# Optimization experiments

Hardware: AMD Instinct MI355X
Metric: run time of the kernel (lower is better)

The kernel has to match this reference:

```python
import jax, jax.numpy as jnp
import numpy as np

B, S, D, H, DH, M = 4, 4096, 1024, 16, 64, 128


def _create_projection_matrix(m, d, seed=0):
    # Block-orthogonal Gaussian projection (FAVOR+), same math as the numpy helper.
    np.random.seed(seed)
    n_block = m // d
    blocks = []
    for _ in range(n_block):
        block = np.random.normal(0, 1, (d, d))
        q, _ = np.linalg.qr(block)
        blocks.append(q.T)
    rem = m - n_block * d
    if rem > 0:
        block = np.random.normal(0, 1, (d, d))
        q, _ = np.linalg.qr(block)
        blocks.append(q.T[:rem])
    proj = np.vstack(blocks)
    multiplier = np.linalg.norm(np.random.normal(0, 1, (m, d)), axis=1)
    return (np.diag(multiplier) @ proj).astype(np.float32)


def setup_inputs() -> dict:
    key = jax.random.key(0)
    ks = jax.random.split(key, 8)
    lim_attn = np.sqrt(6.0 / (D + H * DH)).astype(np.float32)
    lim_out = np.sqrt(6.0 / (H * DH + D)).astype(np.float32)
    head_pos = np.linspace(0.0 + 1.0 / (2.0 * H), 1.0, H, endpoint=False, dtype=np.float32).reshape(1, 1, H, 1)
    return {
        "source_input": jax.random.normal(ks[0], (B, S, D), jnp.float32),
        "pos_ft": jax.random.normal(ks[1], (B, S, D), jnp.float32),
        "pos_ft_slopes": jax.random.normal(ks[2], (B, S, D), jnp.float32),
        "value_weight": jax.random.uniform(ks[3], (D, H, DH), jnp.float32, -lim_attn, lim_attn),
        "pos_ft_weight": jax.random.uniform(ks[4], (D, H, DH), jnp.float32, -lim_attn, lim_attn),
        "pos_ft_scale": jnp.ones((1, 1, H, 1), jnp.float32),
        "pos_ft_offsets": jnp.asarray(head_pos),
        "output_weight": jax.random.uniform(ks[5], (H * DH, D), jnp.float32, -lim_out, lim_out),
        "projection_matrix": jnp.asarray(_create_projection_matrix(M, DH, seed=1234)),
    }


def _fourier_features(x, projection_matrix):
    # x: [b, l, h, d] -> [b, l, h, 2m]
    d = x.shape[-1]
    m = projection_matrix.shape[0]
    data_normalizer = 1.0 / (float(d) ** 0.25)
    ratio = 1.0 / (float(m) ** 0.5)
    xd = jnp.einsum('blhd,md->blhm', data_normalizer * x, projection_matrix)
    xd = jnp.clip(xd, -10000.0, 10000.0)
    return jnp.concatenate([ratio * jnp.sin(xd), ratio * jnp.cos(xd)], axis=-1)


def reference(source_input, pos_ft, pos_ft_slopes, value_weight, pos_ft_weight,
              pos_ft_scale, pos_ft_offsets, output_weight, projection_matrix):
    # Projections
    value = jnp.einsum('bnm,mhd->bnhd', source_input, value_weight)        # [B,S,H,DH]
    pos_proj = jnp.einsum('bnm,mhd->bnhd', pos_ft, pos_ft_weight)          # [B,S,H,DH]
    slope_proj = jnp.einsum('bnm,mhd->bnhd', pos_ft_slopes, pos_ft_weight) # [B,S,H,DH]

    query_pos = pos_ft_scale * pos_proj
    key_pos = query_pos + pos_ft_offsets * (pos_ft_scale * slope_proj)

    # FAVOR fourier random features
    q_prime = _fourier_features(query_pos, projection_matrix)  # [B,S,H,2M]
    k_prime = _fourier_features(key_pos, projection_matrix)    # [B,S,H,2M]

    # Linear attention: O(L) kvs accumulation (non-causal, normalize_attn=False)
    kvs = jnp.einsum('blhm,blhd->bhmd', k_prime, value)         # [B,H,2M,DH]
    av = jnp.einsum('blhm,bhmd->blhd', q_prime, kvs)            # [B,S,H,DH]

    slen = av.shape[1]
    norms = jnp.linalg.norm(slope_proj, axis=-1, keepdims=True) / float(slen)
    av = norms * av

    out = jnp.einsum('bnm,md->bnd', av.reshape(av.shape[0], slen, -1), output_weight)
    # Dropout is identity at inference (training=False)
    return out
```

## Files before the change

kernel.cpp:

```cpp
#include <hip/hip_runtime.h>
#include <math.h>


typedef unsigned short u16;
typedef __attribute__((ext_vector_type(8))) short bf16x8;
typedef __attribute__((ext_vector_type(4))) float floatx4;

__device__ __forceinline__ float bf2f(u16 u) {
  union { unsigned int i; float f; } v; v.i = ((unsigned int)u) << 16; return v.f;
}
__device__ __forceinline__ u16 f2bf(float f) {
  union { float f; unsigned int i; } v; v.f = f;
  unsigned int r = v.i + 0x7fffu + ((v.i >> 16) & 1u);
  return (u16)(r >> 16);
}
__device__ __forceinline__ bool wire_f32(const unsigned* probe) {
  return probe[0] == 0x3F800000u;
}
__device__ __forceinline__ void gload_lds16(const void* g, void* l) {
  __builtin_amdgcn_global_load_lds(
      (const __attribute__((address_space(1))) void*)g,
      (__attribute__((address_space(3))) void*)l, 16, 0, 0);
}

__device__ __forceinline__ void gemm_body(
    const u16* __restrict__ A, int lda, const u16* __restrict__ B, int ldb,
    void* __restrict__ C, long coff, int Klog, int fold, int ofmt, bool f32w,
    long m0, long n0, u16* sA, u16* sB)
{
  const int t = threadIdx.x;
  const int wave = t >> 6, lane = t & 63;
  const int ll = lane & 15, quad = lane >> 4;
  const int wm0 = (wave >> 1) * 64, wn0 = (wave & 1) * 64;
  const int lr = lane >> 2, lc = (lane & 3) * 8;
  floatx4 acc[4][4];
  floatx4 zero = {0.0f, 0.0f, 0.0f, 0.0f};
  #pragma unroll
  for (int i = 0; i < 4; i++)
    #pragma unroll
    for (int j = 0; j < 4; j++) acc[i][j] = zero;

  for (int kc = 0; kc < Klog; kc += 32) {
    int akc = kc, bkc = kc;
    if (fold) {
      akc = (kc < 1024) ? kc : kc - 1024;
      bkc = (kc < 2048) ? kc : kc - 2048;
    }
    #pragma unroll
    for (int j = 0; j < 2; j++) {
      int r0 = wave * 32 + j * 16;
      gload_lds16(&A[(m0 + r0 + lr) * (long)lda + akc + lc], &sA[r0 * 32]);
      gload_lds16(&B[(n0 + r0 + lr) * (long)ldb + bkc + lc], &sB[r0 * 32]);
    }
    __syncthreads();
    bf16x8 af[4], bfr[4];
    #pragma unroll
    for (int i = 0; i < 4; i++) {
      af[i]  = *(const bf16x8*)&sA[(wm0 + i * 16 + ll) * 32 + quad * 8];
      bfr[i] = *(const bf16x8*)&sB[(wn0 + i * 16 + ll) * 32 + quad * 8];
    }
    #pragma unroll
    for (int i = 0; i < 4; i++)
      #pragma unroll
      for (int j = 0; j < 4; j++)
        acc[i][j] = __builtin_amdgcn_mfma_f32_16x16x32_bf16(af[i], bfr[j], acc[i][j], 0, 0, 0);
    __syncthreads();
  }
  #pragma unroll
  for (int i = 0; i < 4; i++)
    #pragma unroll
    for (int j = 0; j < 4; j++)
      #pragma unroll
      for (int r = 0; r < 4; r++) {
        long row = m0 + wm0 + i * 16 + quad * 4 + r;
        long col = n0 + wn0 + j * 16 + ll;
        float v = acc[i][j][r];
        long addr = coff + row * 1024 + col;
        if (ofmt == 0) ((u16*)C)[addr] = f2bf(v);
        else if (ofmt == 1) ((float*)C)[addr] = v;
        else if (f32w) ((float*)C)[addr] = v;
        else ((u16*)C)[addr] = f2bf(v);
      }
}

__global__ __launch_bounds__(256) void gemm_gl(
    const u16* __restrict__ A, int lda, const u16* __restrict__ B, int ldb,
    void* __restrict__ C, long coff, int Klog, int fold, int ofmt,
    const unsigned* __restrict__ probe)
{
  __shared__ u16 sA[128 * 32], sB[128 * 32];
  gemm_body(A, lda, B, ldb, C, coff, Klog, fold, ofmt, wire_f32(probe),
            (long)blockIdx.x * 128, (long)blockIdx.y * 128, sA, sB);
}

__global__ __launch_bounds__(256) void gemm_mega(
    const u16* __restrict__ A2, const u16* __restrict__ W2,
    float* __restrict__ posp, const u16* __restrict__ srcb,
    const u16* __restrict__ wvt, u16* __restrict__ vT,
    const unsigned* __restrict__ probe)
{
  __shared__ u16 pool[20480];
  const int id = blockIdx.x;
  const int xcd = id & 7, pos = id >> 3;
  const int t = threadIdx.x;
  const int wave = t >> 6, lane = t & 63;
  const int ll = lane & 15, quad = lane >> 4;
  const int wm0 = (wave >> 1) * 64, wn0 = (wave & 1) * 64;
  const int lr = lane >> 2, lc = (lane & 3) * 8;
  floatx4 acc[4][4];
  floatx4 zero = {0.0f, 0.0f, 0.0f, 0.0f};
  #pragma unroll
  for (int i = 0; i < 4; i++)
    #pragma unroll
    for (int j = 0; j < 4; j++) acc[i][j] = zero;

  if (pos < 64) {
    int tile = xcd * 64 + pos;
    long m0 = (long)(tile >> 3) * 128, n0 = (long)(tile & 7) * 128;
    u16* sAh = pool;
    u16* sAl = pool + 4096;
    u16* sBh = pool + 8192;
    u16* sBl = pool + 12288;
    for (int kc = 0; kc < 1024; kc += 32) {
      #pragma unroll
      for (int j = 0; j < 2; j++) {
        int r0 = wave * 32 + j * 16;
        gload_lds16(&A2[(m0 + r0 + lr) * 2048 + kc + lc],        &sAh[r0 * 32]);
        gload_lds16(&A2[(m0 + r0 + lr) * 2048 + 1024 + kc + lc], &sAl[r0 * 32]);
        gload_lds16(&W2[(n0 + r0 + lr) * 2048 + kc + lc],        &sBh[r0 * 32]);
        gload_lds16(&W2[(n0 + r0 + lr) * 2048 + 1024 + kc + lc], &sBl[r0 * 32]);
      }
      __syncthreads();
      bf16x8 ah[4], al[4], bh[4], bl[4];
      #pragma unroll
      for (int i = 0; i < 4; i++) {
        ah[i] = *(const bf16x8*)&sAh[(wm0 + i * 16 + ll) * 32 + quad * 8];
        al[i] = *(const bf16x8*)&sAl[(wm0 + i * 16 + ll) * 32 + quad * 8];
        bh[i] = *(const bf16x8*)&sBh[(wn0 + i * 16 + ll) * 32 + quad * 8];
        bl[i] = *(const bf16x8*)&sBl[(wn0 + i * 16 + ll) * 32 + quad * 8];
      }
      #pragma unroll
      for (int i = 0; i < 4; i++)
        #pragma unroll
        for (int j = 0; j < 4; j++) {
          acc[i][j] = __builtin_amdgcn_mfma_f32_16x16x32_bf16(ah[i], bh[j], acc[i][j], 0, 0, 0);
          acc[i][j] = __builtin_amdgcn_mfma_f32_16x16x32_bf16(ah[i], bl[j], acc[i][j], 0, 0, 0);
          acc[i][j] = __builtin_amdgcn_mfma_f32_16x16x32_bf16(al[i], bh[j], acc[i][j], 0, 0, 0);
        }
      __syncthreads();
    }
    #pragma unroll
    for (int i = 0; i < 4; i++)
      #pragma unroll
      for (int j = 0; j < 4; j++)
        #pragma unroll
        for (int r = 0; r < 4; r++) {
          long row = m0 + wm0 + i * 16 + quad * 4 + r;
          long col = n0 + wn0 + j * 16 + ll;
          posp[row * 1024 + col] = acc[i][j][r];
        }
  } else {
    int v = xcd * 32 + (pos - 64);
    long m0 = (long)(v >> 3) * 128, n0 = (long)(v & 7) * 128;
    u16* sA = pool;
    u16* sB = pool + 4096;
    for (int kc = 0; kc < 1024; kc += 32) {
      #pragma unroll
      for (int j = 0; j < 2; j++) {
        int r0 = wave * 32 + j * 16;
        gload_lds16(&srcb[(m0 + r0 + lr) * 1024 + kc + lc], &sA[r0 * 32]);
        gload_lds16(&wvt[(n0 + r0 + lr) * 1024 + kc + lc],  &sB[r0 * 32]);
      }
      __syncthreads();
      bf16x8 af[4], bfr[4];
      #pragma unroll
      for (int i = 0; i < 4; i++) {
        af[i]  = *(const bf16x8*)&sA[(wm0 + i * 16 + ll) * 32 + quad * 8];
        bfr[i] = *(const bf16x8*)&sB[(wn0 + i * 16 + ll) * 32 + quad * 8];
      }
      #pragma unroll
      for (int i = 0; i < 4; i++)
        #pragma unroll
        for (int j = 0; j < 4; j++)
          acc[i][j] = __builtin_amdgcn_mfma_f32_16x16x32_bf16(af[i], bfr[j], acc[i][j], 0, 0, 0);
      __syncthreads();
    }
    u16 (*sT)[136] = (u16(*)[136])pool;
    #pragma unroll
    for (int i = 0; i < 4; i++)
      #pragma unroll
      for (int j = 0; j < 4; j++)
        #pragma unroll
        for (int r = 0; r < 4; r++)
          sT[wn0 + j * 16 + ll][wm0 + i * 16 + quad * 4 + r] = f2bf(acc[i][j][r]);
    __syncthreads();
    for (int u = t; u < 2048; u += 256) {
      int d = u >> 4, c8 = (u & 15) * 8;
      *(uint4*)&vT[(n0 + d) * 4096 + m0 + c8] = *(const uint4*)&sT[d][c8];
    }
  }
}

__device__ __forceinline__ void split_body(
    const void* __restrict__ Aw, long aoff, u16* __restrict__ A2, int rowbase,
    bool f32w, long idx)
{
  int row = (int)(idx >> 7);
  int c8 = (int)(idx & 127) * 8;
  u16 h8[8], l8[8];
  if (f32w) {
    const float* ap = (const float*)Aw + aoff + (long)row * 1024 + c8;
    #pragma unroll
    for (int e = 0; e < 8; e++) {
      float v = ap[e]; u16 hb = f2bf(v);
      h8[e] = hb; l8[e] = f2bf(v - bf2f(hb));
    }
  } else {
    *(uint4*)h8 = *(const uint4*)((const u16*)Aw + aoff + (long)row * 1024 + c8);
    #pragma unroll
    for (int e = 0; e < 8; e++) l8[e] = 0;
  }
  u16* orow = A2 + (long)(rowbase + row) * 2048;
  *(uint4*)&orow[c8] = *(uint4*)h8;
  *(uint4*)&orow[1024 + c8] = *(uint4*)l8;
}

__device__ __forceinline__ void conv_body(
    const void* __restrict__ Aw, long aoff, u16* __restrict__ out,
    bool f32w, long idx)
{
  long base = idx * 8;
  u16 h8[8];
  if (f32w) {
    const float* ap = (const float*)Aw + aoff + base;
    #pragma unroll
    for (int e = 0; e < 8; e++) h8[e] = f2bf(ap[e]);
  } else {
    *(uint4*)h8 = *(const uint4*)((const u16*)Aw + aoff + base);
  }
  *(uint4*)&out[base] = *(uint4*)h8;
}

__global__ __launch_bounds__(256) void split_hilo(
    const void* __restrict__ Aw, long aoff, u16* __restrict__ A2, int rowbase,
    const unsigned* __restrict__ probe)
{
  split_body(Aw, aoff, A2, rowbase, wire_f32(probe),
             (long)blockIdx.x * 256 + threadIdx.x);
}

__global__ __launch_bounds__(256) void conv_bf16(
    const void* __restrict__ Aw, long aoff, u16* __restrict__ out,
    const unsigned* __restrict__ probe)
{
  conv_body(Aw, aoff, out, wire_f32(probe),
            (long)blockIdx.x * 256 + threadIdx.x);
}

__global__ __launch_bounds__(256) void mega2(
    const u16* __restrict__ av, const u16* __restrict__ wot,
    void* __restrict__ dout, long coff,
    const void* __restrict__ posf, const void* __restrict__ slpf,
    const void* __restrict__ src, long ioff_next,
    u16* __restrict__ A2, u16* __restrict__ srcb,
    const unsigned* __restrict__ probe)
{
  __shared__ u16 sA[128 * 32], sB[128 * 32];
  const bool f32w = wire_f32(probe);
  int id = blockIdx.x;
  if (id < 256) {
    int tile = (id & 7) * 32 + (id >> 3);
    gemm_body(av, 1024, wot, 1024, dout, coff, 1024, 0, 2, f32w,
              (long)(tile >> 3) * 128, (long)(tile & 7) * 128, sA, sB);
  } else if (id < 2304) {
    split_body(posf, ioff_next, A2, 0, f32w,
               (long)(id - 256) * 256 + threadIdx.x);
  } else if (id < 4352) {
    split_body(slpf, ioff_next, A2, 4096, f32w,
               (long)(id - 2304) * 256 + threadIdx.x);
  } else {
    conv_body(src, ioff_next, srcb, f32w,
              (long)(id - 4352) * 256 + threadIdx.x);
  }
}

__global__ __launch_bounds__(256) void transpose_w(
    const void* __restrict__ in, u16* __restrict__ outb,
    const unsigned* __restrict__ probe)
{
  __shared__ float s[64][65];
  const bool f32w = wire_f32(probe);
  int t = threadIdx.x;
  int r0 = blockIdx.y * 64, c0 = blockIdx.x * 64;
  for (int u = t; u < 4096; u += 256) {
    int r = u >> 6, c = u & 63;
    long idx = (long)(r0 + r) * 1024 + c0 + c;
    s[c][r] = f32w ? ((const float*)in)[idx] : bf2f(((const u16*)in)[idx]);
  }
  __syncthreads();
  for (int u = t; u < 4096; u += 256) {
    int r = u >> 6, c = u & 63;
    outb[(long)(c0 + r) * 1024 + r0 + c] = f2bf(s[r][c]);
  }
}

__global__ __launch_bounds__(256) void transpose_w2(
    const void* __restrict__ in, u16* __restrict__ out2,
    const unsigned* __restrict__ probe)
{
  __shared__ float s[64][65];
  const bool f32w = wire_f32(probe);
  int t = threadIdx.x;
  int r0 = blockIdx.y * 64, c0 = blockIdx.x * 64;
  for (int u = t; u < 4096; u += 256) {
    int r = u >> 6, c = u & 63;
    long idx = (long)(r0 + r) * 1024 + c0 + c;
    s[c][r] = f32w ? ((const float*)in)[idx] : bf2f(((const u16*)in)[idx]);
  }
  __syncthreads();
  for (int u = t; u < 4096; u += 256) {
    int r = u >> 6, c = u & 63;
    float v = s[r][c];
    u16 hb = f2bf(v);
    long rowb = (long)(c0 + r) * 2048;
    out2[rowb + r0 + c] = hb;
    out2[rowb + 1024 + r0 + c] = f2bf(v - bf2f(hb));
  }
}

__global__ __launch_bounds__(256) void proj_prep(
    const void* __restrict__ proj, u16* __restrict__ P2,
    const unsigned* __restrict__ probe)
{
  const bool f32w = wire_f32(probe);
  int idx = blockIdx.x * 256 + threadIdx.x;
  int m = idx >> 6, d = idx & 63;
  const float dn = 0.3535533905932738f;
  float v = dn * (f32w ? ((const float*)proj)[idx] : bf2f(((const u16*)proj)[idx]));
  u16 hb = f2bf(v);
  P2[(long)m * 128 + d] = hb;
  P2[(long)m * 128 + 64 + d] = f2bf(v - bf2f(hb));
}

__global__ __launch_bounds__(256) void featurize_mfma(
    const float* __restrict__ posp, const float* __restrict__ slpp,
    const u16* __restrict__ P2, const void* __restrict__ scl,
    const void* __restrict__ offs, u16* __restrict__ qp, u16* __restrict__ kpT,
    const unsigned* __restrict__ probe, int h0)
{
  __shared__ u16 sAp[4 * 64 * 32], sAs[4 * 64 * 32], sB[4 * 128 * 32];
  const bool f32w = wire_f32(probe);
  const int t = threadIdx.x;
  const int wave = t >> 6, lane = t & 63;
  const int ll = lane & 15, quad = lane >> 4;
  const int wm0 = (wave >> 1) * 32, wn0 = (wave & 1) * 64;
  const int g = blockIdx.y, h = h0 + g;
  const int l0 = blockIdx.x * 64;
  const float s1 = f32w ? ((const float*)scl)[h] : bf2f(((const u16*)scl)[h]);
  const float s2 = (f32w ? ((const float*)offs)[h] : bf2f(((const u16*)offs)[h])) * s1;
  const float ratio = 0.08838834764831845f;

  for (int u = t; u < 512; u += 256) {
    int r = u >> 3, cc = u & 7;
    const float* pp = posp + (long)(l0 + r) * 1024 + h * 64 + cc * 8;
    const float* sp = slpp + (long)(l0 + r) * 1024 + h * 64 + cc * 8;
    u16 ph[8], pl[8], sh[8], sl[8];
    #pragma unroll
    for (int e = 0; e < 8; e++) {
      float vp = pp[e]; u16 hb = f2bf(vp);
      ph[e] = hb; pl[e] = f2bf(vp - bf2f(hb));
      float vs = sp[e]; u16 sb = f2bf(vs);
      sh[e] = sb; sl[e] = f2bf(vs - bf2f(sb));
    }
    int ch = cc >> 2, cw = (cc & 3) * 8;
    *(uint4*)&sAp[((ch) * 64 + r) * 32 + cw]     = *(uint4*)ph;
    *(uint4*)&sAp[((2 + ch) * 64 + r) * 32 + cw] = *(uint4*)pl;
    *(uint4*)&sAs[((ch) * 64 + r) * 32 + cw]     = *(uint4*)sh;
    *(uint4*)&sAs[((2 + ch) * 64 + r) * 32 + cw] = *(uint4*)sl;
  }
  for (int u = t; u < 2048; u += 256) {
    int r = u >> 4, q4 = u & 15;
    uint4 v = *(const uint4*)&P2[(long)r * 128 + q4 * 8];
    int ch = q4 >> 2, cw = (q4 & 3) * 8;
    *(uint4*)&sB[(ch * 128 + r) * 32 + cw] = v;
  }
  __syncthreads();

  floatx4 accp[2][4], accs[2][4];
  floatx4 zero = {0.0f, 0.0f, 0.0f, 0.0f};
  #pragma unroll
  for (int i = 0; i < 2; i++)
    #pragma unroll
    for (int j = 0; j < 4; j++) { accp[i][j] = zero; accs[i][j] = zero; }

  const int ACH[6] = {0, 1, 0, 1, 2, 3};
  const int BCH[6] = {0, 1, 2, 3, 0, 1};
  #pragma unroll
  for (int kci = 0; kci < 6; kci++) {
    int ac = ACH[kci], bc = BCH[kci];
    bf16x8 ap[2], as2[2], bfr[4];
    #pragma unroll
    for (int i = 0; i < 2; i++) {
      ap[i]  = *(const bf16x8*)&sAp[(ac * 64 + wm0 + i * 16 + ll) * 32 + quad * 8];
      as2[i] = *(const bf16x8*)&sAs[(ac * 64 + wm0 + i * 16 + ll) * 32 + quad * 8];
    }
    #pragma unroll
    for (int j = 0; j < 4; j++)
      bfr[j] = *(const bf16x8*)&sB[(bc * 128 + wn0 + j * 16 + ll) * 32 + quad * 8];
    #pragma unroll
    for (int i = 0; i < 2; i++)
      #pragma unroll
      for (int j = 0; j < 4; j++) {
        accp[i][j] = __builtin_amdgcn_mfma_f32_16x16x32_bf16(ap[i],  bfr[j], accp[i][j], 0, 0, 0);
        accs[i][j] = __builtin_amdgcn_mfma_f32_16x16x32_bf16(as2[i], bfr[j], accs[i][j], 0, 0, 0);
      }
  }

  #pragma unroll
  for (int i = 0; i < 2; i++) {
    int lbase = l0 + wm0 + i * 16 + quad * 4;
    #pragma unroll
    for (int j = 0; j < 4; j++) {
      int m = wn0 + j * 16 + ll;
      u16 ksin[4], kcos[4];
      #pragma unroll
      for (int r = 0; r < 4; r++) {
        float dq = s1 * accp[i][j][r];
        float dk = dq + s2 * accs[i][j][r];
        dq = fminf(fmaxf(dq, -10000.0f), 10000.0f);
        dk = fminf(fmaxf(dk, -10000.0f), 10000.0f);
        long qbase = ((long)g * 4096 + lbase + r) * 256;
        qp[qbase + m]       = f2bf(ratio * __sinf(dq));
        qp[qbase + m + 128] = f2bf(ratio * __cosf(dq));
        ksin[r] = f2bf(ratio * __sinf(dk));
        kcos[r] = f2bf(ratio * __cosf(dk));
      }
      *(uint2*)&kpT[((long)(g * 256 + m)) * 4096 + lbase]       = *(uint2*)ksin;
      *(uint2*)&kpT[((long)(g * 256 + m + 128)) * 4096 + lbase] = *(uint2*)kcos;
    }
  }
}

__global__ __launch_bounds__(256) void transpose_v(
    const u16* __restrict__ in, u16* __restrict__ out)
{
  __shared__ u16 s[64][72];
  int t = threadIdx.x;
  int c0 = blockIdx.x * 64;
  int r0 = blockIdx.y * 64;
  for (int u = t; u < 512; u += 256) {
    int r = u >> 3, c8 = (u & 7) * 8;
    uint4 v = *(const uint4*)&in[(long)(r0 + r) * 1024 + c0 + c8];
    const u16* pv = (const u16*)&v;
    #pragma unroll
    for (int e = 0; e < 8; e++) s[c8 + e][r] = pv[e];
  }
  __syncthreads();
  for (int u = t; u < 512; u += 256) {
    int r = u >> 3, c8 = (u & 7) * 8;
    *(uint4*)&out[(long)(c0 + r) * 4096 + r0 + c8] = *(const uint4*)&s[r][c8];
  }
}

__global__ __launch_bounds__(256) void norm_kernel(
    const float* __restrict__ slp, float* __restrict__ nrm)
{
  int idx = blockIdx.x * 256 + threadIdx.x;
  int row = idx >> 4, h = idx & 15;
  const float* p = slp + (long)row * 1024 + h * 64;
  float acc = 0.0f;
  #pragma unroll
  for (int i = 0; i < 16; i++) {
    float4 v = *(const float4*)&p[i * 4];
    acc += v.x * v.x + v.y * v.y + v.z * v.z + v.w * v.w;
  }
  nrm[idx] = sqrtf(acc) * (1.0f / 4096.0f);
}

__global__ __launch_bounds__(256) void kvs_mfma(
    const u16* __restrict__ kpT, const u16* __restrict__ vT,
    float* __restrict__ kvp, int h0)
{
  __shared__ u16 sA[256][40], sB[64][40];
  const int t = threadIdx.x;
  const int wave = t >> 6, lane = t & 63;
  const int ll = lane & 15, quad = lane >> 4;
  const int wm0 = wave * 64;
  const int ks = blockIdx.x, g = blockIdx.y;
  const int G = gridDim.y, KS = gridDim.x;
  const int h = h0 + g;
  const int lch = 4096 / KS;
  const int lbase = ks * lch;
  floatx4 acc[4][4];
  floatx4 zero = {0.0f, 0.0f, 0.0f, 0.0f};
  #pragma unroll
  for (int i = 0; i < 4; i++)
    #pragma unroll
    for (int j = 0; j < 4; j++) acc[i][j] = zero;

  for (int kc = 0; kc < lch; kc += 32) {
    for (int u = t; u < 1024; u += 256) {
      int r = u >> 2, s = u & 3;
      *(uint4*)&sA[r][s * 8] =
          *(const uint4*)&kpT[((long)(g * 256 + r)) * 4096 + lbase + kc + s * 8];
    }
    {
      int r = t >> 2, s = t & 3;
      if (t < 256)
        *(uint4*)&sB[r][s * 8] =
            *(const uint4*)&vT[((long)(h * 64 + r)) * 4096 + lbase + kc + s * 8];
    }
    __syncthreads();
    bf16x8 af[4], bfr[4];
    #pragma unroll
    for (int i = 0; i < 4; i++) {
      af[i] = *(const bf16x8*)&sA[wm0 + i * 16 + ll][quad * 8];
      bfr[i] = *(const bf16x8*)&sB[i * 16 + ll][quad * 8];
    }
    #pragma unroll
    for (int i = 0; i < 4; i++)
      #pragma unroll
      for (int j = 0; j < 4; j++)
        acc[i][j] = __builtin_amdgcn_mfma_f32_16x16x32_bf16(af[i], bfr[j], acc[i][j], 0, 0, 0);
    __syncthreads();
  }
  long obase = ((long)ks * G + g) * 256;
  #pragma unroll
  for (int i = 0; i < 4; i++)
    #pragma unroll
    for (int j = 0; j < 4; j++)
      #pragma unroll
      for (int r = 0; r < 4; r++) {
        int row = wm0 + i * 16 + quad * 4 + r;
        int col = j * 16 + ll;
        kvp[(obase + row) * 64 + col] = acc[i][j][r];
      }
}

__global__ __launch_bounds__(256) void kvs_reduce(
    const float* __restrict__ kvp, u16* __restrict__ kvsTh,
    u16* __restrict__ kvsTl, int G, int KS)
{
  int idx = blockIdx.x * 256 + threadIdx.x;
  int m = idx & 255, d = (idx >> 8) & 63, g = idx >> 14;
  float s = 0.0f;
  for (int p = 0; p < KS; p++)
    s += kvp[(((long)p * G + g) * 256 + m) * 64 + d];
  u16 hb = f2bf(s);
  long o = ((long)g * 64 + d) * 256 + m;
  kvsTh[o] = hb;
  kvsTl[o] = f2bf(s - bf2f(hb));
}

__global__ __launch_bounds__(256) void av_mfma(
    const u16* __restrict__ qp, const u16* __restrict__ kvsTh,
    const u16* __restrict__ kvsTl, const float* __restrict__ nrm,
    u16* __restrict__ av, int h0)
{
  __shared__ u16 sA[128][40], sBh[64][40], sBl[64][40];
  const int t = threadIdx.x;
  const int wave = t >> 6, lane = t & 63;
  const int ll = lane & 15, quad = lane >> 4;
  const int wm0 = wave * 32;
  const int g = blockIdx.y, h = h0 + g;
  const int l0 = blockIdx.x * 128;
  floatx4 acc[2][4];
  floatx4 zero = {0.0f, 0.0f, 0.0f, 0.0f};
  #pragma unroll
  for (int i = 0; i < 2; i++)
    #pragma unroll
    for (int j = 0; j < 4; j++) acc[i][j] = zero;

  for (int kc = 0; kc < 256; kc += 32) {
    for (int u = t; u < 512; u += 256) {
      int r = u >> 2, s = u & 3;
      *(uint4*)&sA[r][s * 8] =
          *(const uint4*)&qp[((long)g * 4096 + l0 + r) * 256 + kc + s * 8];
    }
    {
      int r = t >> 2, s4 = t & 3;
      long o = ((long)g * 64 + r) * 256 + kc + s4 * 8;
      *(uint4*)&sBh[r][s4 * 8] = *(const uint4*)&kvsTh[o];
      *(uint4*)&sBl[r][s4 * 8] = *(const uint4*)&kvsTl[o];
    }
    __syncthreads();
    bf16x8 af[2], bh[4], bl[4];
    #pragma unroll
    for (int i = 0; i < 2; i++)
      af[i] = *(const bf16x8*)&sA[wm0 + i * 16 + ll][quad * 8];
    #pragma unroll
    for (int j = 0; j < 4; j++) {
      bh[j] = *(const bf16x8*)&sBh[j * 16 + ll][quad * 8];
      bl[j] = *(const bf16x8*)&sBl[j * 16 + ll][quad * 8];
    }
    #pragma unroll
    for (int i = 0; i < 2; i++)
      #pragma unroll
      for (int j = 0; j < 4; j++) {
        acc[i][j] = __builtin_amdgcn_mfma_f32_16x16x32_bf16(af[i], bh[j], acc[i][j], 0, 0, 0);
        acc[i][j] = __builtin_amdgcn_mfma_f32_16x16x32_bf16(af[i], bl[j], acc[i][j], 0, 0, 0);
      }
    __syncthreads();
  }
  #pragma unroll
  for (int i = 0; i < 2; i++)
    #pragma unroll
    for (int r = 0; r < 4; r++) {
      int l = l0 + wm0 + i * 16 + quad * 4 + r;
      float nv = nrm[l * 16 + h];
      #pragma unroll
      for (int j = 0; j < 4; j++) {
        int d = j * 16 + ll;
        av[(long)l * 1024 + h * 64 + d] = f2bf(acc[i][j][r] * nv);
      }
    }
}

extern "C" void kernel_launch(void* const* d_in, const int* in_sizes, int n_in,
                              void* d_out, int out_size, void* d_ws, size_t ws_size,
                              hipStream_t stream) {
  const void* src  = d_in[0];
  const void* posf = d_in[1];
  const void* slpf = d_in[2];
  const void* wv   = d_in[3];
  const void* wp   = d_in[4];
  const void* scl  = d_in[5];
  const void* offs = d_in[6];
  const void* wo   = d_in[7];
  const void* proj = d_in[8];
  const unsigned* probe = (const unsigned*)d_in[5];
  char* ws = (char*)d_ws;
  const size_t KiB = 1024;
  const size_t MiB = 1024 * 1024;

  u16*   wvt   = (u16*)(ws + 0 * MiB);
  u16*   wot   = (u16*)(ws + 2 * MiB);
  u16*   W2    = (u16*)(ws + 4 * MiB);
  float* nrm   = (float*)(ws + 8 * MiB);
  u16*   P2    = (u16*)(ws + 8 * MiB + 256 * KiB);
  u16*   kvsTh = (u16*)(ws + 8 * MiB + 320 * KiB);
  u16*   kvsTl = (u16*)(ws + 8 * MiB + 832 * KiB);
  float* posp  = (float*)(ws + 10 * MiB);
  float* slpp  = (float*)(ws + 26 * MiB);
  u16*   valb  = (u16*)(ws + 42 * MiB);
  u16*   av    = valb;
  u16*   vT    = (u16*)(ws + 50 * MiB);
  char*  dyn   = ws + 58 * MiB;

  const int KS = 16;
  int G = 1;
  int stacked = 0;
  if (ws_size >= 122 * MiB) { G = 16; stacked = 1; }
  else if (ws_size >= 92 * MiB) { G = 4; stacked = 1; }
  u16* qp  = (u16*)dyn;
  u16* kpT = (u16*)(dyn + 2 * (size_t)G * MiB);
  u16* A2  = (u16*)dyn;
  u16* srcb = (G == 16) ? kpT : (u16*)dyn;
  float* kvp = (G == 16) ? posp : (float*)(dyn + 4 * (size_t)G * MiB);

  dim3 blk(256);
  transpose_w<<<dim3(16, 16), blk, 0, stream>>>(wv, wvt, probe);
  transpose_w<<<dim3(16, 16), blk, 0, stream>>>(wo, wot, probe);
  transpose_w2<<<dim3(16, 16), blk, 0, stream>>>(wp, W2, probe);
  proj_prep<<<dim3(32), blk, 0, stream>>>(proj, P2, probe);

  if (G == 16) {
    split_hilo<<<dim3(2048), blk, 0, stream>>>(posf, 0, A2, 0, probe);
    split_hilo<<<dim3(2048), blk, 0, stream>>>(slpf, 0, A2, 4096, probe);
    conv_bf16<<<dim3(2048), blk, 0, stream>>>(src, 0, srcb, probe);
    for (int b = 0; b < 4; b++) {
      long ioff = (long)b * 4096 * 1024;
      gemm_mega<<<dim3(768), blk, 0, stream>>>(A2, W2, posp, srcb, wvt, vT, probe);
      norm_kernel<<<dim3(256), blk, 0, stream>>>(slpp, nrm);
      featurize_mfma<<<dim3(64, 16), blk, 0, stream>>>(
          posp, slpp, P2, scl, offs, qp, kpT, probe, 0);
      kvs_mfma<<<dim3(KS, 16), blk, 0, stream>>>(kpT, vT, kvp, 0);
      kvs_reduce<<<dim3(16 * 64), blk, 0, stream>>>(kvp, kvsTh, kvsTl, 16, KS);
      av_mfma<<<dim3(32, 16), blk, 0, stream>>>(qp, kvsTh, kvsTl, nrm, av, 0);
      if (b < 3) {
        long ioff_n = (long)(b + 1) * 4096 * 1024;
        mega2<<<dim3(6400), blk, 0, stream>>>(av, wot, d_out, ioff,
                                              posf, slpf, src, ioff_n,
                                              A2, srcb, probe);
      } else {
        gemm_gl<<<dim3(32, 8), blk, 0, stream>>>(av, 1024, wot, 1024,
                                                 d_out, ioff, 1024, 0, 2, probe);
      }
    }
  } else {
    for (int b = 0; b < 4; b++) {
      long ioff = (long)b * 4096 * 1024;
      if (stacked) {
        split_hilo<<<dim3(2048), blk, 0, stream>>>(posf, ioff, A2, 0, probe);
        split_hilo<<<dim3(2048), blk, 0, stream>>>(slpf, ioff, A2, 4096, probe);
        gemm_gl<<<dim3(64, 8), blk, 0, stream>>>(A2, 2048, W2, 2048,
                                                 posp, 0, 3072, 1, 1, probe);
      } else {
        split_hilo<<<dim3(2048), blk, 0, stream>>>(posf, ioff, A2, 0, probe);
        gemm_gl<<<dim3(32, 8), blk, 0, stream>>>(A2, 2048, W2, 2048,
                                                 posp, 0, 3072, 1, 1, probe);
        split_hilo<<<dim3(2048), blk, 0, stream>>>(slpf, ioff, A2, 0, probe);
        gemm_gl<<<dim3(32, 8), blk, 0, stream>>>(A2, 2048, W2, 2048,
                                                 slpp, 0, 3072, 1, 1, probe);
      }
      norm_kernel<<<dim3(256), blk, 0, stream>>>(slpp, nrm);
      conv_bf16<<<dim3(2048), blk, 0, stream>>>(src, ioff, srcb, probe);
      gemm_gl<<<dim3(32, 8), blk, 0, stream>>>(srcb, 1024, wvt, 1024,
                                               valb, 0, 1024, 0, 0, probe);
      transpose_v<<<dim3(16, 64), blk, 0, stream>>>(valb, vT);
      for (int hg = 0; hg < 16; hg += G) {
        featurize_mfma<<<dim3(64, G), blk, 0, stream>>>(
            posp, slpp, P2, scl, offs, qp, kpT, probe, hg);
        kvs_mfma<<<dim3(KS, G), blk, 0, stream>>>(kpT, vT, kvp, hg);
        kvs_reduce<<<dim3(G * 64), blk, 0, stream>>>(kvp, kvsTh, kvsTl, G, KS);
        av_mfma<<<dim3(32, G), blk, 0, stream>>>(qp, kvsTh, kvsTl, nrm, av, hg);
      }
      gemm_gl<<<dim3(32, 8), blk, 0, stream>>>(av, 1024, wot, 1024,
                                               d_out, ioff, 1024, 0, 2, probe);
    }
  }
}
```

Measured before the change: 936.4 us.

## Stage featurize and av epilogue outputs through LDS for coalesced stores; fuse prep kernels

Result: no change. 936.4 us (+0.0%).

```diff
diff --git a/kernel.cpp b/kernel.cpp
--- a/kernel.cpp
+++ b/kernel.cpp
@@ -255,6 +255,22 @@
 {
   conv_body(Aw, aoff, out, wire_f32(probe),
             (long)blockIdx.x * 256 + threadIdx.x);
+}
+
+__global__ __launch_bounds__(256) void stage3(
+    const void* __restrict__ posf, const void* __restrict__ slpf,
+    const void* __restrict__ src, long ioff,
+    u16* __restrict__ A2, u16* __restrict__ srcb,
+    const unsigned* __restrict__ probe)
+{
+  const bool f32w = wire_f32(probe);
+  int id = blockIdx.x;
+  if (id < 2048)
+    split_body(posf, ioff, A2, 0, f32w, (long)id * 256 + threadIdx.x);
+  else if (id < 4096)
+    split_body(slpf, ioff, A2, 4096, f32w, (long)(id - 2048) * 256 + threadIdx.x);
+  else
+    conv_body(src, ioff, srcb, f32w, (long)(id - 4096) * 256 + threadIdx.x);
 }
 
 __global__ __launch_bounds__(256) void mega2(
@@ -348,7 +364,10 @@
     const void* __restrict__ offs, u16* __restrict__ qp, u16* __restrict__ kpT,
     const unsigned* __restrict__ probe, int h0)
 {
-  __shared__ u16 sAp[4 * 64 * 32], sAs[4 * 64 * 32], sB[4 * 128 * 32];
+  __shared__ u16 pool[35328];
+  u16* sAp = pool;
+  u16* sAs = pool + 8192;
+  u16* sB  = pool + 16384;
   const bool f32w = wire_f32(probe);
   const int t = threadIdx.x;
   const int wave = t >> 6, lane = t & 63;
@@ -416,28 +435,38 @@
       }
   }
 
+  u16* sq = pool;
+  u16* sk = pool + 64 * 264;
+  __syncthreads();
   #pragma unroll
   for (int i = 0; i < 2; i++) {
-    int lbase = l0 + wm0 + i * 16 + quad * 4;
+    int lrow = wm0 + i * 16 + quad * 4;
     #pragma unroll
     for (int j = 0; j < 4; j++) {
       int m = wn0 + j * 16 + ll;
-      u16 ksin[4], kcos[4];
       #pragma unroll
       for (int r = 0; r < 4; r++) {
         float dq = s1 * accp[i][j][r];
         float dk = dq + s2 * accs[i][j][r];
         dq = fminf(fmaxf(dq, -10000.0f), 10000.0f);
         dk = fminf(fmaxf(dk, -10000.0f), 10000.0f);
-        long qbase = ((long)g * 4096 + lbase + r) * 256;
-        qp[qbase + m]       = f2bf(ratio * __sinf(dq));
-        qp[qbase + m + 128] = f2bf(ratio * __cosf(dq));
-        ksin[r] = f2bf(ratio * __sinf(dk));
-        kcos[r] = f2bf(ratio * __cosf(dk));
-      }
-      *(uint2*)&kpT[((long)(g * 256 + m)) * 4096 + lbase]       = *(uint2*)ksin;
-      *(uint2*)&kpT[((long)(g * 256 + m + 128)) * 4096 + lbase] = *(uint2*)kcos;
-    }
+        sq[(lrow + r) * 264 + m]       = f2bf(ratio * __sinf(dq));
+        sq[(lrow + r) * 264 + 128 + m] = f2bf(ratio * __cosf(dq));
+        sk[m * 72 + lrow + r]          = f2bf(ratio * __sinf(dk));
+        sk[(m + 128) * 72 + lrow + r]  = f2bf(ratio * __cosf(dk));
+      }
+    }
+  }
+  __syncthreads();
+  for (int u = t; u < 2048; u += 256) {
+    int rrow = u >> 5, c8 = (u & 31) * 8;
+    *(uint4*)&qp[((long)g * 4096 + l0 + rrow) * 256 + c8] =
+        *(const uint4*)&sq[rrow * 264 + c8];
+  }
+  for (int u = t; u < 2048; u += 256) {
+    int mrow = u >> 3, c8 = (u & 7) * 8;
+    *(uint4*)&kpT[((long)(g * 256 + mrow)) * 4096 + l0 + c8] =
+        *(const uint4*)&sk[mrow * 72 + c8];
   }
 }
 
@@ -557,7 +586,10 @@
     const u16* __restrict__ kvsTl, const float* __restrict__ nrm,
     u16* __restrict__ av, int h0)
 {
-  __shared__ u16 sA[128][40], sBh[64][40], sBl[64][40];
+  __shared__ u16 pool[10240];
+  u16* sA  = pool;
+  u16* sBh = pool + 5120;
+  u16* sBl = pool + 7680;
   const int t = threadIdx.x;
   const int wave = t >> 6, lane = t & 63;
   const int ll = lane & 15, quad = lane >> 4;
@@ -574,24 +606,24 @@
   for (int kc = 0; kc < 256; kc += 32) {
     for (int u = t; u < 512; u += 256) {
       int r = u >> 2, s = u & 3;
-      *(uint4*)&sA[r][s * 8] =
+      *(uint4*)&sA[r * 40 + s * 8] =
           *(const uint4*)&qp[((long)g * 4096 + l0 + r) * 256 + kc + s * 8];
     }
     {
       int r = t >> 2, s4 = t & 3;
       long o = ((long)g * 64 + r) * 256 + kc + s4 * 8;
-      *(uint4*)&sBh[r][s4 * 8] = *(const uint4*)&kvsTh[o];
-      *(uint4*)&sBl[r][s4 * 8] = *(const uint4*)&kvsTl[o];
+      *(uint4*)&sBh[r * 40 + s4 * 8] = *(const uint4*)&kvsTh[o];
+      *(uint4*)&sBl[r * 40 + s4 * 8] = *(const uint4*)&kvsTl[o];
     }
     __syncthreads();
     bf16x8 af[2], bh[4], bl[4];
     #pragma unroll
     for (int i = 0; i < 2; i++)
-      af[i] = *(const bf16x8*)&sA[wm0 + i * 16 + ll][quad * 8];
+      af[i] = *(const bf16x8*)&sA[(wm0 + i * 16 + ll) * 40 + quad * 8];
     #pragma unroll
     for (int j = 0; j < 4; j++) {
-      bh[j] = *(const bf16x8*)&sBh[j * 16 + ll][quad * 8];
-      bl[j] = *(const bf16x8*)&sBl[j * 16 + ll][quad * 8];
+      bh[j] = *(const bf16x8*)&sBh[(j * 16 + ll) * 40 + quad * 8];
+      bl[j] = *(const bf16x8*)&sBl[(j * 16 + ll) * 40 + quad * 8];
     }
     #pragma unroll
     for (int i = 0; i < 2; i++)
@@ -602,18 +634,23 @@
       }
     __syncthreads();
   }
+  u16* sT = pool;
   #pragma unroll
   for (int i = 0; i < 2; i++)
     #pragma unroll
     for (int r = 0; r < 4; r++) {
-      int l = l0 + wm0 + i * 16 + quad * 4 + r;
-      float nv = nrm[l * 16 + h];
-      #pragma unroll
-      for (int j = 0; j < 4; j++) {
-        int d = j * 16 + ll;
-        av[(long)l * 1024 + h * 64 + d] = f2bf(acc[i][j][r] * nv);
-      }
-    }
+      int lrow = wm0 + i * 16 + quad * 4 + r;
+      float nv = nrm[(l0 + lrow) * 16 + h];
+      #pragma unroll
+      for (int j = 0; j < 4; j++)
+        sT[lrow * 72 + j * 16 + ll] = f2bf(acc[i][j][r] * nv);
+    }
+  __syncthreads();
+  for (int u = t; u < 1024; u += 256) {
+    int lrow = u >> 3, c8 = (u & 7) * 8;
+    *(uint4*)&av[(long)(l0 + lrow) * 1024 + h * 64 + c8] =
+        *(const uint4*)&sT[lrow * 72 + c8];
+  }
 }
 
 extern "C" void kernel_launch(void* const* d_in, const int* in_sizes, int n_in,
@@ -665,9 +702,7 @@
   proj_prep<<<dim3(32), blk, 0, stream>>>(proj, P2, probe);
 
   if (G == 16) {
-    split_hilo<<<dim3(2048), blk, 0, stream>>>(posf, 0, A2, 0, probe);
-    split_hilo<<<dim3(2048), blk, 0, stream>>>(slpf, 0, A2, 4096, probe);
-    conv_bf16<<<dim3(2048), blk, 0, stream>>>(src, 0, srcb, probe);
+    stage3<<<dim3(6144), blk, 0, stream>>>(posf, slpf, src, 0, A2, srcb, probe);
     for (int b = 0; b < 4; b++) {
       long ioff = (long)b * 4096 * 1024;
       gemm_mega<<<dim3(768), blk, 0, stream>>>(A2, W2, posp, srcb, wvt, vT, probe);
```
